# Optimization experiments

Measured on AMD Instinct MI355X. Metric: run time of the kernel, lower is better.

The kernel has to match this reference:

```python
import jax, jax.numpy as jnp
import numpy as np

N_HEADS = 16
HEAD_DIM = 128  # dim // n_heads = 2048 // 16

def setup_inputs() -> dict:
    key = jax.random.key(0)
    ks = jax.random.split(key, 7)
    B, S, D = 2, 2048, 2048
    scale = 0.02
    return {
        "q": jax.random.normal(ks[0], (B, S, D), dtype=jnp.float32),
        "k": jax.random.normal(ks[1], (B, S, D), dtype=jnp.float32),
        "v": jax.random.normal(ks[2], (B, S, D), dtype=jnp.float32),
        "wq": jax.random.normal(ks[3], (D, D), dtype=jnp.float32) * scale,
        "wk": jax.random.normal(ks[4], (D, D), dtype=jnp.float32) * scale,
        "wv": jax.random.normal(ks[5], (D, D), dtype=jnp.float32) * scale,
        "wo": jax.random.normal(ks[6], (D, D), dtype=jnp.float32) * scale,
    }

def reference(q, k, v, wq, wk, wv, wo):
    B, S, _ = q.shape
    # Linear (no bias): torch Linear computes x @ W.T; weights here stored as [out, in]
    xq = (q @ wq.T).reshape(B, S, N_HEADS, HEAD_DIM).transpose(0, 2, 1, 3)  # [B,H,S,d]
    xk = (k @ wk.T).reshape(B, S, N_HEADS, HEAD_DIM).transpose(0, 2, 1, 3)
    xv = (v @ wv.T).reshape(B, S, N_HEADS, HEAD_DIM).transpose(0, 2, 1, 3)
    scores = jnp.einsum("bhqd,bhkd->bhqk", xq, xk) / jnp.sqrt(jnp.float32(HEAD_DIM))
    # causal mask: -inf above the diagonal
    causal = jnp.tril(jnp.ones((S, S), dtype=bool))
    scores = jnp.where(causal[None, None], scores, -jnp.inf)
    attn = jax.nn.softmax(scores.astype(jnp.float32), axis=-1)  # dropout is identity at eval
    out = jnp.einsum("bhqk,bhkd->bhqd", attn, xv)
    out = out.transpose(0, 2, 1, 3).reshape(B, S, N_HEADS * HEAD_DIM)
    return out @ wo.T
```

## Files before the change

### kernel.cpp

```cpp
#include <hip/hip_runtime.h>
#include <hip/hip_bf16.h>

#define B_ 2
#define S_ 2048
#define D_ 2048
#define H_ 16
#define HD_ 128

typedef __attribute__((ext_vector_type(4))) float f32x4;
typedef __attribute__((ext_vector_type(8))) short bf16x8;

static __device__ __forceinline__ unsigned short f2bf(float f) {
    unsigned int u = __float_as_uint(f);
    u += 0x7fffu + ((u >> 16) & 1u);
    return (unsigned short)(u >> 16);
}
static __device__ __forceinline__ float bf2f(unsigned short h) {
    return __uint_as_float(((unsigned int)h) << 16);
}

#define MFMA_K32(a, b, c) __builtin_amdgcn_mfma_f32_16x16x32_bf16(a, b, c, 0, 0, 0)

static __device__ __forceinline__ void gll16(const void* g, void* l) {
    __builtin_amdgcn_global_load_lds((const __attribute__((address_space(1))) void*)g,
                                     (__attribute__((address_space(3))) void*)l,
                                     16, 0, 0);
}

__global__ void cvt_in(const float4* __restrict__ src, ushort4* __restrict__ dst) {
    int i = blockIdx.x * 256 + threadIdx.x;
    float4 v = src[i];
    ushort4 o;
    o.x = f2bf(v.x); o.y = f2bf(v.y); o.z = f2bf(v.z); o.w = f2bf(v.w);
    dst[i] = o;
}

__global__ void cvt_w4(const float4* __restrict__ s0, ushort4* __restrict__ d0,
                       const float4* __restrict__ s1, ushort4* __restrict__ d1,
                       const float4* __restrict__ s2, ushort4* __restrict__ d2,
                       const float4* __restrict__ s3, ushort4* __restrict__ d3) {
    const float4* s; ushort4* d;
    switch (blockIdx.y) {
        case 0: s = s0; d = d0; break;
        case 1: s = s1; d = d1; break;
        case 2: s = s2; d = d2; break;
        default: s = s3; d = d3; break;
    }
    int i = blockIdx.x * 256 + threadIdx.x;
    float4 v = s[i];
    ushort4 o;
    o.x = f2bf(v.x); o.y = f2bf(v.y); o.z = f2bf(v.z); o.w = f2bf(v.w);
    d[i] = o;
}

template<int OUT_MODE>
__global__ __launch_bounds__(256) void gemm_xwt(
        const unsigned short* __restrict__ A,
        const unsigned short* __restrict__ W,
        void* __restrict__ C) {
    constexpr int K = D_;
    __shared__ unsigned short As[2][128 * 32];
    __shared__ unsigned short Ws[2][128 * 32];
    const int tid = threadIdx.x, lane = tid & 63, wid = tid >> 6;
    const int wy = wid >> 1, wx = wid & 1;
    const int g = lane >> 4, lr = lane & 15;
    const int swz = (blockIdx.x & 7) * 64 + (blockIdx.x >> 3);
    const int bm = (swz & 31) * 128;
    const int bn = (swz >> 5) * 128;

    const int r0 = (wid * 128 + lane) >> 2, c0 = (lane & 3) * 8;
    const int r1 = r0 + 16;

    f32x4 acc[4][4] = {};

    auto stage = [&](int k0, int nb) {
        gll16(A + (size_t)(bm + r0) * K + k0 + c0, (char*)&As[nb][0] + wid * 2048);
        gll16(A + (size_t)(bm + r1) * K + k0 + c0, (char*)&As[nb][0] + wid * 2048 + 1024);
        gll16(W + (size_t)(bn + r0) * K + k0 + c0, (char*)&Ws[nb][0] + wid * 2048);
        gll16(W + (size_t)(bn + r1) * K + k0 + c0, (char*)&Ws[nb][0] + wid * 2048 + 1024);
    };

    stage(0, 0);
    int cur = 0;

    for (int k0 = 0; k0 < K; k0 += 32) {
        __syncthreads();
        if (k0 + 32 < K) stage(k0 + 32, cur ^ 1);
        bf16x8 af[4], wf[4];
        #pragma unroll
        for (int i = 0; i < 4; ++i)
            af[i] = *(const bf16x8*)((const char*)&As[cur][0] + (wy * 64 + i * 16 + lr) * 64 + g * 16);
        #pragma unroll
        for (int i = 0; i < 4; ++i)
            wf[i] = *(const bf16x8*)((const char*)&Ws[cur][0] + (wx * 64 + i * 16 + lr) * 64 + g * 16);
        #pragma unroll
        for (int mi = 0; mi < 4; ++mi)
            #pragma unroll
            for (int ni = 0; ni < 4; ++ni)
                acc[mi][ni] = MFMA_K32(af[mi], wf[ni], acc[mi][ni]);
        cur ^= 1;
    }

    #pragma unroll
    for (int mi = 0; mi < 4; ++mi) {
        #pragma unroll
        for (int ni = 0; ni < 4; ++ni) {
            const int n = bn + wx * 64 + ni * 16 + lr;
            const int m0 = bm + wy * 64 + mi * 16 + g * 4;
            if constexpr (OUT_MODE == 0) {
                #pragma unroll
                for (int rg = 0; rg < 4; ++rg) {
                    int m = m0 + rg;
                    int bb = m >> 11, s = m & (S_ - 1);
                    int hh = n >> 7, dd = n & (HD_ - 1);
                    ((unsigned short*)C)[(((size_t)(bb * H_ + hh) * S_) + s) * HD_ + dd] =
                        f2bf(acc[mi][ni][rg]);
                }
            } else if constexpr (OUT_MODE == 1) {
                #pragma unroll
                for (int rg = 0; rg < 4; ++rg) {
                    int m = m0 + rg;
                    int bb = m >> 11, s = m & (S_ - 1);
                    int hh = n >> 7, dd = n & (HD_ - 1);
                    int vr = s & 63;
                    int pr = (vr & 3) | (((vr >> 3) & 3) << 2) | (((vr >> 2) & 1) << 4) | (vr & 32);
                    size_t eo = ((size_t)(bb * H_ + hh) << 18) + ((size_t)(s >> 6) << 13)
                              + pr * 128 + (((((unsigned)dd) << 1) ^ ((pr & 7) << 4)) >> 1);
                    ((unsigned short*)C)[eo] = f2bf(acc[mi][ni][rg]);
                }
            } else if constexpr (OUT_MODE == 2) {
                int bb = m0 >> 11, s0 = m0 & (S_ - 1);
                int hh = n >> 7, dd = n & (HD_ - 1);
                int ch = ((s0 & 63) >> 3) ^ (dd & 7);
                size_t eo = ((size_t)(bb * H_ + hh) << 18) + ((size_t)(s0 >> 6) << 13)
                          + dd * 64 + (ch << 3) + (s0 & 7);
                ushort4 pk;
                pk.x = f2bf(acc[mi][ni][0]); pk.y = f2bf(acc[mi][ni][1]);
                pk.z = f2bf(acc[mi][ni][2]); pk.w = f2bf(acc[mi][ni][3]);
                *(ushort4*)&((unsigned short*)C)[eo] = pk;
            } else {
                #pragma unroll
                for (int rg = 0; rg < 4; ++rg)
                    ((float*)C)[(size_t)(m0 + rg) * D_ + n] = acc[mi][ni][rg];
            }
        }
    }
}

__global__ __launch_bounds__(256) void attn_fwd(
        const unsigned short* __restrict__ Qg,
        const unsigned short* __restrict__ Kt,
        const unsigned short* __restrict__ Vt,
        unsigned short* __restrict__ Og) {
    __shared__ char Ks[2][16384];
    __shared__ char Vs[2][16384];
    const int tid = threadIdx.x, lane = tid & 63, w = tid >> 6;
    const int g = lane >> 4, lr = lane & 15;
    const int i = blockIdx.x;
    const int hi = i >> 8, j = i & 255;
    const int bh = j & 31;
    const int p = j >> 5;
    const int qt = hi ? p : 15 - p;
    const int b = bh >> 4, h = bh & (H_ - 1);
    const size_t base = (size_t)bh * S_ * HD_;
    const float SCL = 0.08838834764831845f * 1.4426950408889634f;

    auto stage = [&](int t, int nb) {
        const size_t tb = base + (size_t)t * 8192 + w * 2048 + (size_t)lane * 8;
        char* kd = &Ks[nb][0] + w * 4096;
        char* vd = &Vs[nb][0] + w * 4096;
        gll16(Kt + tb, kd);               gll16(Kt + tb + 512, kd + 1024);
        gll16(Kt + tb + 1024, kd + 2048); gll16(Kt + tb + 1536, kd + 3072);
        gll16(Vt + tb, vd);               gll16(Vt + tb + 512, vd + 1024);
        gll16(Vt + tb + 1024, vd + 2048); gll16(Vt + tb + 1536, vd + 3072);
    };

    const int q0 = qt * 128;
    const int qrA = q0 + w * 16 + lr, qrB = qrA + 64;

    bf16x8 qfA[4], qfB[4];
    #pragma unroll
    for (int st = 0; st < 4; ++st) {
        bf16x8 ta = *(const bf16x8*)(Qg + base + (size_t)qrA * HD_ + st * 32 + g * 8);
        bf16x8 tb2 = *(const bf16x8*)(Qg + base + (size_t)qrB * HD_ + st * 32 + g * 8);
        #pragma unroll
        for (int jj = 0; jj < 8; ++jj) {
            ta[jj] = (short)f2bf(bf2f((unsigned short)ta[jj]) * SCL);
            tb2[jj] = (short)f2bf(bf2f((unsigned short)tb2[jj]) * SCL);
        }
        qfA[st] = ta; qfB[st] = tb2;
    }

    float mA = -1e30f, lA = 0.0f, mB = -1e30f, lB = 0.0f;
    f32x4 accA[8] = {}, accB[8] = {};
    const int nt = 2 * qt + 2;

    stage(0, 0);
    int cur = 0;

    for (int t = 0; t < nt; ++t) {
        __syncthreads();
        if (t + 1 < nt) stage(t + 1, cur ^ 1);
        const char* Kb = &Ks[cur][0];
        const char* Vb = &Vs[cur][0];
        const bool actA = (t < nt - 1);

        f32x4 sA[4] = {}, sB[4] = {};
        __builtin_amdgcn_s_setprio(1);
        #pragma unroll
        for (int f = 0; f < 4; ++f) {
            const int row = f * 16 + lr;
            const int sw = (row & 7) << 4;
            #pragma unroll
            for (int st = 0; st < 4; ++st) {
                bf16x8 kf = *(const bf16x8*)(Kb + row * 256 + ((st * 64 + g * 16) ^ sw));
                if (actA) sA[f] = MFMA_K32(kf, qfA[st], sA[f]);
                sB[f] = MFMA_K32(kf, qfB[st], sB[f]);
            }
        }
        __builtin_amdgcn_s_setprio(0);

        if (t == nt - 2) {
            #pragma unroll
            for (int f = 0; f < 4; ++f)
                #pragma unroll
                for (int rg = 0; rg < 4; ++rg)
                    if (q0 + 32 * (f >> 1) + 8 * g + 4 * (f & 1) + rg > qrA)
                        sA[f][rg] = -1e30f;
        }
        if (t == nt - 1) {
            #pragma unroll
            for (int f = 0; f < 4; ++f)
                #pragma unroll
                for (int rg = 0; rg < 4; ++rg)
                    if (q0 + 64 + 32 * (f >> 1) + 8 * g + 4 * (f & 1) + rg > qrB)
                        sB[f][rg] = -1e30f;
        }

        bf16x8 pAlo, pAhi, pBlo, pBhi;
        auto softmax_step = [&](f32x4* sf, float& m_r, float& l_r, f32x4* accO,
                                bf16x8& plo, bf16x8& phi) {
            float pm = -1e30f;
            #pragma unroll
            for (int f = 0; f < 4; ++f)
                #pragma unroll
                for (int rg = 0; rg < 4; ++rg) pm = fmaxf(pm, sf[f][rg]);
            pm = fmaxf(pm, __shfl_xor(pm, 16));
            pm = fmaxf(pm, __shfl_xor(pm, 32));
            if (!__all(pm <= m_r + 8.0f)) {
                const float mnew = fmaxf(m_r, pm);
                const float corr = exp2f(m_r - mnew);
                m_r = mnew;
                float cj[4];
                #pragma unroll
                for (int jj = 0; jj < 4; ++jj) cj[jj] = __shfl(corr, g * 4 + jj);
                #pragma unroll
                for (int db = 0; db < 8; ++db) {
                    accO[db][0] *= cj[0]; accO[db][1] *= cj[1];
                    accO[db][2] *= cj[2]; accO[db][3] *= cj[3];
                }
                l_r *= corr;
            }
            float ls = 0.0f;
            #pragma unroll
            for (int f = 0; f < 2; ++f)
                #pragma unroll
                for (int rg = 0; rg < 4; ++rg) {
                    float pv = exp2f(sf[f][rg] - m_r);
                    ls += pv;
                    plo[f * 4 + rg] = (short)f2bf(pv);
                }
            #pragma unroll
            for (int f = 0; f < 2; ++f)
                #pragma unroll
                for (int rg = 0; rg < 4; ++rg) {
                    float pv = exp2f(sf[2 + f][rg] - m_r);
                    ls += pv;
                    phi[f * 4 + rg] = (short)f2bf(pv);
                }
            ls += __shfl_xor(ls, 16);
            ls += __shfl_xor(ls, 32);
            l_r += ls;
        };
        if (actA) softmax_step(sA, mA, lA, accA, pAlo, pAhi);
        softmax_step(sB, mB, lB, accB, pBlo, pBhi);

        __builtin_amdgcn_s_setprio(1);
        #pragma unroll
        for (int db = 0; db < 8; ++db) {
            const int d = db * 16 + lr;
            bf16x8 vlo = *(const bf16x8*)(Vb + d * 128 + ((g ^ (d & 7)) << 4));
            bf16x8 vhi = *(const bf16x8*)(Vb + d * 128 + (((4 + g) ^ (d & 7)) << 4));
            if (actA) {
                accA[db] = MFMA_K32(pAlo, vlo, accA[db]);
                accA[db] = MFMA_K32(pAhi, vhi, accA[db]);
            }
            accB[db] = MFMA_K32(pBlo, vlo, accB[db]);
            accB[db] = MFMA_K32(pBhi, vhi, accB[db]);
        }
        __builtin_amdgcn_s_setprio(0);
        cur ^= 1;
    }

    {
        float lj[4];
        #pragma unroll
        for (int jj = 0; jj < 4; ++jj) lj[jj] = __shfl(lA, g * 4 + jj);
        #pragma unroll
        for (int jj = 0; jj < 4; ++jj) {
            const int qq = q0 + w * 16 + g * 4 + jj;
            const float inv = 1.0f / lj[jj];
            unsigned short* dst = Og + ((size_t)(b * S_ + qq)) * D_ + h * HD_;
            #pragma unroll
            for (int db = 0; db < 8; ++db)
                dst[db * 16 + lr] = f2bf(accA[db][jj] * inv);
        }
        #pragma unroll
        for (int jj = 0; jj < 4; ++jj) lj[jj] = __shfl(lB, g * 4 + jj);
        #pragma unroll
        for (int jj = 0; jj < 4; ++jj) {
            const int qq = q0 + 64 + w * 16 + g * 4 + jj;
            const float inv = 1.0f / lj[jj];
            unsigned short* dst = Og + ((size_t)(b * S_ + qq)) * D_ + h * HD_;
            #pragma unroll
            for (int db = 0; db < 8; ++db)
                dst[db * 16 + lr] = f2bf(accB[db][jj] * inv);
        }
    }
}

extern "C" void kernel_launch(void* const* d_in, const int* in_sizes, int n_in,
                              void* d_out, int out_size, void* d_ws, size_t ws_size,
                              hipStream_t stream) {
    const float* q  = (const float*)d_in[0];
    const float* k  = (const float*)d_in[1];
    const float* v  = (const float*)d_in[2];
    const float* wq = (const float*)d_in[3];
    const float* wk = (const float*)d_in[4];
    const float* wv = (const float*)d_in[5];
    const float* wo = (const float*)d_in[6];

    unsigned short* ws   = (unsigned short*)d_ws;
    unsigned short* wqb  = ws;
    unsigned short* wkb  = wqb + (size_t)D_ * D_;
    unsigned short* wvb  = wkb + (size_t)D_ * D_;
    unsigned short* wob  = wvb + (size_t)D_ * D_;
    unsigned short* xq   = wob + (size_t)D_ * D_;
    unsigned short* xk   = xq + (size_t)B_ * S_ * D_;
    unsigned short* xv   = xk + (size_t)B_ * S_ * D_;
    unsigned short* slot = xv + (size_t)B_ * S_ * D_;

    cvt_w4<<<dim3(4096, 4), 256, 0, stream>>>(
        (const float4*)wq, (ushort4*)wqb, (const float4*)wk, (ushort4*)wkb,
        (const float4*)wv, (ushort4*)wvb, (const float4*)wo, (ushort4*)wob);

    cvt_in<<<8192, 256, 0, stream>>>((const float4*)q, (ushort4*)slot);
    gemm_xwt<0><<<512, 256, 0, stream>>>(slot, wqb, xq);
    cvt_in<<<8192, 256, 0, stream>>>((const float4*)k, (ushort4*)slot);
    gemm_xwt<1><<<512, 256, 0, stream>>>(slot, wkb, xk);
    cvt_in<<<8192, 256, 0, stream>>>((const float4*)v, (ushort4*)slot);
    gemm_xwt<2><<<512, 256, 0, stream>>>(slot, wvb, xv);

    attn_fwd<<<512, 256, 0, stream>>>(xq, xk, xv, slot);

    gemm_xwt<3><<<512, 256, 0, stream>>>(slot, wob, d_out);
}
```

Before: 344.4 us.

## Shrink attention blocks to 64 query rows with single-buffered KV staging

```diff
diff --git a/kernel.cpp b/kernel.cpp
--- a/kernel.cpp
+++ b/kernel.cpp
@@ -147,36 +147,36 @@
     }
 }
 
-__global__ __launch_bounds__(256) void attn_fwd(
+__global__ __launch_bounds__(128, 4) void attn_fwd(
         const unsigned short* __restrict__ Qg,
         const unsigned short* __restrict__ Kt,
         const unsigned short* __restrict__ Vt,
         unsigned short* __restrict__ Og) {
-    __shared__ char Ks[2][16384];
-    __shared__ char Vs[2][16384];
+    __shared__ char Ks[16384];
+    __shared__ char Vs[16384];
     const int tid = threadIdx.x, lane = tid & 63, w = tid >> 6;
     const int g = lane >> 4, lr = lane & 15;
     const int i = blockIdx.x;
-    const int hi = i >> 8, j = i & 255;
-    const int bh = j & 31;
-    const int p = j >> 5;
-    const int qt = hi ? p : 15 - p;
+    const int qi = 31 - (i >> 5);
+    const int bh = i & 31;
     const int b = bh >> 4, h = bh & (H_ - 1);
     const size_t base = (size_t)bh * S_ * HD_;
     const float SCL = 0.08838834764831845f * 1.4426950408889634f;
 
-    auto stage = [&](int t, int nb) {
-        const size_t tb = base + (size_t)t * 8192 + w * 2048 + (size_t)lane * 8;
-        char* kd = &Ks[nb][0] + w * 4096;
-        char* vd = &Vs[nb][0] + w * 4096;
-        gll16(Kt + tb, kd);               gll16(Kt + tb + 512, kd + 1024);
-        gll16(Kt + tb + 1024, kd + 2048); gll16(Kt + tb + 1536, kd + 3072);
-        gll16(Vt + tb, vd);               gll16(Vt + tb + 512, vd + 1024);
-        gll16(Vt + tb + 1024, vd + 2048); gll16(Vt + tb + 1536, vd + 3072);
+    auto stage = [&](int t) {
+        const size_t tb = base + (size_t)t * 8192 + w * 4096 + (size_t)lane * 8;
+        char* kd = Ks + w * 8192;
+        char* vd = Vs + w * 8192;
+        #pragma unroll
+        for (int c = 0; c < 8; ++c) {
+            gll16(Kt + tb + c * 512, kd + c * 1024);
+            gll16(Vt + tb + c * 512, vd + c * 1024);
+        }
     };
 
-    const int q0 = qt * 128;
-    const int qrA = q0 + w * 16 + lr, qrB = qrA + 64;
+    const int q0 = qi * 64;
+    const int qrA = q0 + w * 16 + lr;
+    const int qrB = qrA + 32;
 
     bf16x8 qfA[4], qfB[4];
     #pragma unroll
@@ -193,17 +193,12 @@
 
     float mA = -1e30f, lA = 0.0f, mB = -1e30f, lB = 0.0f;
     f32x4 accA[8] = {}, accB[8] = {};
-    const int nt = 2 * qt + 2;
-
-    stage(0, 0);
-    int cur = 0;
+    const int nt = qi + 1;
 
     for (int t = 0; t < nt; ++t) {
         __syncthreads();
-        if (t + 1 < nt) stage(t + 1, cur ^ 1);
-        const char* Kb = &Ks[cur][0];
-        const char* Vb = &Vs[cur][0];
-        const bool actA = (t < nt - 1);
+        stage(t);
+        __syncthreads();
 
         f32x4 sA[4] = {}, sB[4] = {};
         __builtin_amdgcn_s_setprio(1);
@@ -213,28 +208,22 @@
             const int sw = (row & 7) << 4;
             #pragma unroll
             for (int st = 0; st < 4; ++st) {
-                bf16x8 kf = *(const bf16x8*)(Kb + row * 256 + ((st * 64 + g * 16) ^ sw));
-                if (actA) sA[f] = MFMA_K32(kf, qfA[st], sA[f]);
+                bf16x8 kf = *(const bf16x8*)(Ks + row * 256 + ((st * 64 + g * 16) ^ sw));
+                sA[f] = MFMA_K32(kf, qfA[st], sA[f]);
                 sB[f] = MFMA_K32(kf, qfB[st], sB[f]);
             }
         }
         __builtin_amdgcn_s_setprio(0);
 
-        if (t == nt - 2) {
+        if (t == nt - 1) {
             #pragma unroll
             for (int f = 0; f < 4; ++f)
                 #pragma unroll
-                for (int rg = 0; rg < 4; ++rg)
-                    if (q0 + 32 * (f >> 1) + 8 * g + 4 * (f & 1) + rg > qrA)
-                        sA[f][rg] = -1e30f;
-        }
-        if (t == nt - 1) {
-            #pragma unroll
-            for (int f = 0; f < 4; ++f)
-                #pragma unroll
-                for (int rg = 0; rg < 4; ++rg)
-                    if (q0 + 64 + 32 * (f >> 1) + 8 * g + 4 * (f & 1) + rg > qrB)
-                        sB[f][rg] = -1e30f;
+                for (int rg = 0; rg < 4; ++rg) {
+                    const int kv = q0 + 32 * (f >> 1) + 8 * g + 4 * (f & 1) + rg;
+                    if (kv > qrA) sA[f][rg] = -1e30f;
+                    if (kv > qrB) sB[f][rg] = -1e30f;
+                }
         }
 
         bf16x8 pAlo, pAhi, pBlo, pBhi;
@@ -282,24 +271,21 @@
             ls += __shfl_xor(ls, 32);
             l_r += ls;
         };
-        if (actA) softmax_step(sA, mA, lA, accA, pAlo, pAhi);
+        softmax_step(sA, mA, lA, accA, pAlo, pAhi);
         softmax_step(sB, mB, lB, accB, pBlo, pBhi);
 
         __builtin_amdgcn_s_setprio(1);
         #pragma unroll
         for (int db = 0; db < 8; ++db) {
             const int d = db * 16 + lr;
-            bf16x8 vlo = *(const bf16x8*)(Vb + d * 128 + ((g ^ (d & 7)) << 4));
-            bf16x8 vhi = *(const bf16x8*)(Vb + d * 128 + (((4 + g) ^ (d & 7)) << 4));
-            if (actA) {
-                accA[db] = MFMA_K32(pAlo, vlo, accA[db]);
-                accA[db] = MFMA_K32(pAhi, vhi, accA[db]);
-            }
+            bf16x8 vlo = *(const bf16x8*)(Vs + d * 128 + ((g ^ (d & 7)) << 4));
+            bf16x8 vhi = *(const bf16x8*)(Vs + d * 128 + (((4 + g) ^ (d & 7)) << 4));
+            accA[db] = MFMA_K32(pAlo, vlo, accA[db]);
+            accA[db] = MFMA_K32(pAhi, vhi, accA[db]);
             accB[db] = MFMA_K32(pBlo, vlo, accB[db]);
             accB[db] = MFMA_K32(pBhi, vhi, accB[db]);
         }
         __builtin_amdgcn_s_setprio(0);
-        cur ^= 1;
     }
 
     {
@@ -319,7 +305,7 @@
         for (int jj = 0; jj < 4; ++jj) lj[jj] = __shfl(lB, g * 4 + jj);
         #pragma unroll
         for (int jj = 0; jj < 4; ++jj) {
-            const int qq = q0 + 64 + w * 16 + g * 4 + jj;
+            const int qq = q0 + 32 + w * 16 + g * 4 + jj;
             const float inv = 1.0f / lj[jj];
             unsigned short* dst = Og + ((size_t)(b * S_ + qq)) * D_ + h * HD_;
             #pragma unroll
@@ -361,7 +347,7 @@
     cvt_in<<<8192, 256, 0, stream>>>((const float4*)v, (ushort4*)slot);
     gemm_xwt<2><<<512, 256, 0, stream>>>(slot, wvb, xv);
 
-    attn_fwd<<<512, 256, 0, stream>>>(xq, xk, xv, slot);
+    attn_fwd<<<1024, 128, 0, stream>>>(xq, xk, xv, slot);
 
     gemm_xwt<3><<<512, 256, 0, stream>>>(slot, wob, d_out);
 }
```

Result: slower. 358.5 us (+4.1%).

## Prefetch two stages ahead with explicit vmcnt waits in GEMM and attention

Applied to the files above, without the earlier changes.

```diff
diff --git a/kernel.cpp b/kernel.cpp
--- a/kernel.cpp
+++ b/kernel.cpp
@@ -20,6 +20,7 @@
 }
 
 #define MFMA_K32(a, b, c) __builtin_amdgcn_mfma_f32_16x16x32_bf16(a, b, c, 0, 0, 0)
+#define FENCE() asm volatile("" ::: "memory")
 
 static __device__ __forceinline__ void gll16(const void* g, void* l) {
     __builtin_amdgcn_global_load_lds((const __attribute__((address_space(1))) void*)g,
@@ -81,11 +82,14 @@
     };
 
     stage(0, 0);
+    stage(32, 1);
     int cur = 0;
 
     for (int k0 = 0; k0 < K; k0 += 32) {
-        __syncthreads();
-        if (k0 + 32 < K) stage(k0 + 32, cur ^ 1);
+        if (k0 + 32 < K) asm volatile("s_waitcnt vmcnt(4)" ::: "memory");
+        else             asm volatile("s_waitcnt vmcnt(0)" ::: "memory");
+        __builtin_amdgcn_s_barrier();
+        FENCE();
         bf16x8 af[4], wf[4];
         #pragma unroll
         for (int i = 0; i < 4; ++i)
@@ -98,6 +102,10 @@
             #pragma unroll
             for (int ni = 0; ni < 4; ++ni)
                 acc[mi][ni] = MFMA_K32(af[mi], wf[ni], acc[mi][ni]);
+        FENCE();
+        __builtin_amdgcn_s_barrier();
+        FENCE();
+        if (k0 + 64 < K) stage(k0 + 64, cur);
         cur ^= 1;
     }
 
@@ -157,26 +165,29 @@
     const int tid = threadIdx.x, lane = tid & 63, w = tid >> 6;
     const int g = lane >> 4, lr = lane & 15;
     const int i = blockIdx.x;
-    const int hi = i >> 8, j = i & 255;
-    const int bh = j & 31;
-    const int p = j >> 5;
-    const int qt = hi ? p : 15 - p;
+    const int qt = 15 - (i >> 5);
+    const int bh = i & 31;
     const int b = bh >> 4, h = bh & (H_ - 1);
     const size_t base = (size_t)bh * S_ * HD_;
     const float SCL = 0.08838834764831845f * 1.4426950408889634f;
 
     auto stage = [&](int t, int nb) {
-        const size_t tb = base + (size_t)t * 8192 + w * 2048 + (size_t)lane * 8;
+        const char* ksrc = (const char*)Kt + ((size_t)bh << 19) + (size_t)t * 16384
+                         + w * 4096 + (size_t)lane * 16;
+        const char* vsrc = (const char*)Vt + ((size_t)bh << 19) + (size_t)t * 16384
+                         + w * 4096 + (size_t)lane * 16;
         char* kd = &Ks[nb][0] + w * 4096;
         char* vd = &Vs[nb][0] + w * 4096;
-        gll16(Kt + tb, kd);               gll16(Kt + tb + 512, kd + 1024);
-        gll16(Kt + tb + 1024, kd + 2048); gll16(Kt + tb + 1536, kd + 3072);
-        gll16(Vt + tb, vd);               gll16(Vt + tb + 512, vd + 1024);
-        gll16(Vt + tb + 1024, vd + 2048); gll16(Vt + tb + 1536, vd + 3072);
+        #pragma unroll
+        for (int c = 0; c < 4; ++c) {
+            gll16(ksrc + c * 1024, kd + c * 1024);
+            gll16(vsrc + c * 1024, vd + c * 1024);
+        }
     };
 
     const int q0 = qt * 128;
-    const int qrA = q0 + w * 16 + lr, qrB = qrA + 64;
+    const int qrA = q0 + w * 16 + lr;
+    const int qrB = qrA + 64;
 
     bf16x8 qfA[4], qfB[4];
     #pragma unroll
@@ -196,11 +207,14 @@
     const int nt = 2 * qt + 2;
 
     stage(0, 0);
+    stage(1, 1);
     int cur = 0;
 
     for (int t = 0; t < nt; ++t) {
-        __syncthreads();
-        if (t + 1 < nt) stage(t + 1, cur ^ 1);
+        if (t < nt - 1) asm volatile("s_waitcnt vmcnt(8)" ::: "memory");
+        else            asm volatile("s_waitcnt vmcnt(0)" ::: "memory");
+        __builtin_amdgcn_s_barrier();
+        FENCE();
         const char* Kb = &Ks[cur][0];
         const char* Vb = &Vs[cur][0];
         const bool actA = (t < nt - 1);
@@ -299,6 +313,11 @@
             accB[db] = MFMA_K32(pBhi, vhi, accB[db]);
         }
         __builtin_amdgcn_s_setprio(0);
+
+        FENCE();
+        __builtin_amdgcn_s_barrier();
+        FENCE();
+        if (t + 2 < nt) stage(t + 2, cur);
         cur ^= 1;
     }
 
```

Measured after the change: 398.0 us. 1.16x slower.
